# Kernel optimization log

Hardware: AMD Instinct MI355X
Metric: run time of the kernel (lower is better)

## Reference

```python
import math
import jax, jax.numpy as jnp
import numpy as np

ROPE_DIMS = 16  # rope applied to last 16 channels only
N_WIN = 16      # sliding window size


def rmsnorm(x, w):
    return x * jax.lax.rsqrt(jnp.mean(x * x, axis=-1, keepdims=True) + 1e-8) * w


def apply_rope(x, negate=False):
    # x: [B, H, T, C]; rotate last ROPE_DIMS channels with interleaved pairs
    T = x.shape[2]
    x_pass, x_rope = x[..., :-ROPE_DIMS], x[..., -ROPE_DIMS:]
    t = jnp.arange(T, dtype=x.dtype)
    if negate:
        t = -t
    k = jnp.arange(ROPE_DIMS // 2, dtype=x.dtype)
    theta = 10000.0 ** (-2.0 * k / ROPE_DIMS)          # [8]
    freqs = t[:, None] * theta[None, :]                 # [T, 8]
    cos, sin = jnp.cos(freqs), jnp.sin(freqs)
    x1, x2 = x_rope[..., 0::2], x_rope[..., 1::2]
    rx1 = x1 * cos - x2 * sin
    rx2 = x1 * sin + x2 * cos
    rx = jnp.stack([rx1, rx2], axis=-1).reshape(x_rope.shape)
    return jnp.concatenate([x_pass, rx], axis=-1)


def setup_inputs() -> dict:
    key = jax.random.key(0)
    ks = jax.random.split(key, 14)
    B, T, d, c, nh = 4, 2048, 256, 64, 4
    s = 0.02
    return {
        "H": jax.random.normal(ks[0], (B, T, d), jnp.float32),
        "W_Q": jax.random.normal(ks[1], (nh * c, d), jnp.float32) * s,
        "W_K": jax.random.normal(ks[2], (c, d), jnp.float32) * s,
        "W_V": jax.random.normal(ks[3], (c, d), jnp.float32) * s,
        "wq": 1.0 + 0.1 * jax.random.normal(ks[4], (nh, c), jnp.float32),
        "wk": 1.0 + 0.1 * jax.random.normal(ks[5], (c,), jnp.float32),
        "wv": 1.0 + 0.1 * jax.random.normal(ks[6], (c,), jnp.float32),
        "Wg0": jax.random.normal(ks[7], (64, 2 * c), jnp.float32) * s,
        "bg0": jnp.zeros((64,), jnp.float32),
        "Wg1": jax.random.normal(ks[8], (64, 2 * c), jnp.float32) * s,
        "bg1": jnp.zeros((64,), jnp.float32),
        "Wout": jax.random.normal(ks[9], (d, 128), jnp.float32) * s,
        "bout": jnp.zeros((d,), jnp.float32),
    }


def reference(H, W_Q, W_K, W_V, wq, wk, wv, Wg0, bg0, Wg1, bg1, Wout, bout):
    B, T, d = H.shape
    nh, c = wq.shape
    # projections
    Q = (H @ W_Q.T).reshape(B, T, nh, c).transpose(0, 2, 1, 3)   # [B,nh,T,c]
    K = (H @ W_K.T)[:, None]                                      # [B,1,T,c]
    V = (H @ W_V.T)[:, None]                                      # [B,1,T,c]
    # per-head RMSNorm on Q, shared RMSNorm on K/V
    Q = rmsnorm(Q, wq[None, :, None, :])
    K = rmsnorm(K, wk)
    V = rmsnorm(V, wv)
    # partial RoPE (last 16 dims); V is also rotated in this module
    Q = apply_rope(Q)
    K = apply_rope(K)[:, 0]                                       # [B,T,c]
    V = apply_rope(V)[:, 0]
    # dense scores with sliding-window causal mask (width N_WIN)
    S = jnp.einsum('bhtc,bsc->bhts', Q, K) / math.sqrt(c)
    i = jnp.arange(T)[:, None]
    j = jnp.arange(T)[None, :]
    allowed = (j <= i) & (j >= i - (N_WIN - 1))                   # [T,T]
    S = jnp.where(allowed, S, -jnp.inf)
    P = jax.nn.softmax(S, axis=-1)
    O = jnp.einsum('bhts,bsc->bhtc', P, V)                        # [B,nh,T,c]
    O = apply_rope(O, negate=True)
    # group heads {0,1} and {2,3}
    O_g0 = O[:, :2].transpose(0, 2, 1, 3).reshape(B, T, 2 * c)
    O_g1 = O[:, 2:].transpose(0, 2, 1, 3).reshape(B, T, 2 * c)
    p0 = O_g0 @ Wg0.T + bg0
    p1 = O_g1 @ Wg1.T + bg1
    p_all = jnp.concatenate([p0, p1], axis=-1)                    # [B,T,128]
    return p_all @ Wout.T + bout
```

## Files before the change

### kernel.cpp

```cpp
#include <hip/hip_runtime.h>
#include <math.h>

#define T_SEQ 2048
#define DMODEL 256
#define C_HEAD 64
#define NH 4
#define NWIN 16
#define B_SZ 4

typedef __attribute__((ext_vector_type(8))) short bf16x8;
typedef __attribute__((ext_vector_type(8))) unsigned short ushort8;
typedef __attribute__((ext_vector_type(4))) float f32x4;

static __device__ __forceinline__ unsigned short f2bf(float f) {
    union { float f; unsigned int u; } v; v.f = f;
    unsigned int r = v.u + 0x7FFFu + ((v.u >> 16) & 1u);
    return (unsigned short)(r >> 16);
}

__global__ __launch_bounds__(256) void conv_w_kernel(
    const float* __restrict__ WQ, const float* __restrict__ WK,
    const float* __restrict__ WV, const float* __restrict__ Wg0,
    const float* __restrict__ Wg1, const float* __restrict__ Wout,
    unsigned short* __restrict__ dst, float2* __restrict__ rtab) {
    const int tid = threadIdx.x;
    if (blockIdx.x >= 72) {
        const int idx = (blockIdx.x - 72) * 256 + tid;
        const int t = idx >> 3, k = idx & 7;
        const float theta = powf(10000.0f, -0.125f * (float)k);
        const float fr = (float)t * theta;
        rtab[idx] = make_float2(cosf(fr), sinf(fr));
        return;
    }
    const int i = blockIdx.x * 256 + tid;
    const float* s; long off; long doff;
    if (i < 12288) {
        const long e = (long)i * 8;
        const int col = (int)(e >> 8), k = (int)(e & 255);
        if      (col < 256) { s = WQ; off = (long)col * 256 + k; }
        else if (col < 320) { s = WK; off = (long)(col - 256) * 256 + k; }
        else                { s = WV; off = (long)(col - 320) * 256 + k; }
        doff = ((long)(col >> 4) * 8 + (k >> 5)) * 512 + ((k >> 3) & 3) * 128 + (col & 15) * 8;
    } else {
        const long e = (long)(i - 12288) * 8;
        const int col = (int)(e >> 7), k = (int)(e & 127);
        if      (col < 64)  { s = Wg0; off = (long)col * 128 + k; }
        else if (col < 128) { s = Wg1; off = (long)(col - 64) * 128 + k; }
        else                { s = Wout; off = (long)(col - 128) * 128 + k; }
        doff = 98304 + ((long)(col >> 4) * 4 + (k >> 5)) * 512 + ((k >> 3) & 3) * 128 + (col & 15) * 8;
    }
    const float4* s4 = (const float4*)(s + off);
    float4 a = s4[0], b = s4[1];
    ushort8 o;
    o[0] = f2bf(a.x); o[1] = f2bf(a.y); o[2] = f2bf(a.z); o[3] = f2bf(a.w);
    o[4] = f2bf(b.x); o[5] = f2bf(b.y); o[6] = f2bf(b.z); o[7] = f2bf(b.w);
    *(ushort8*)(dst + doff) = o;
}

__global__ __launch_bounds__(512) void fused_kernel(
    const float* __restrict__ H, const unsigned short* __restrict__ Wallb,
    const float* __restrict__ wq, const float* __restrict__ wk,
    const float* __restrict__ wv, const float2* __restrict__ rtab,
    const float* __restrict__ bg0, const float* __restrict__ bg1,
    const float* __restrict__ bout, float* __restrict__ out)
{
    __shared__ __align__(16) char smem[36864];
    char* lds_a = smem;
    char* o_lds = smem;
    char* p_lds = smem + 8192;
    char* q_lds = smem + 16384;
    char* k_lds = smem + 24576;
    char* v_lds = smem + 28672;
    char* p_att = smem + 32768;

    const int tid = threadIdx.x;
    const int blk = blockIdx.x;
    const int b  = blk >> 7;
    const int t0 = (blk & 127) << 4;

    const unsigned short* Wpk2 = Wallb + 98304;

    for (int idx = tid; idx < 1024; idx += 512) {
        int row = idx >> 5, ch = idx & 31;
        int t = t0 - 16 + row; if (t < 0) t = 0;
        const float4* s4 = (const float4*)(H + ((size_t)b * T_SEQ + t) * DMODEL + ch * 8);
        float4 a = s4[0], c = s4[1];
        ushort8 o;
        o[0] = f2bf(a.x); o[1] = f2bf(a.y); o[2] = f2bf(a.z); o[3] = f2bf(a.w);
        o[4] = f2bf(c.x); o[5] = f2bf(c.y); o[6] = f2bf(c.z); o[7] = f2bf(c.w);
        int byte = row * 512 + ch * 16;
        byte ^= (row & 7) << 4;
        *(ushort8*)(lds_a + byte) = o;
    }
    __syncthreads();

    const int w  = tid >> 6;
    const int l  = tid & 63;
    const int g  = l >> 4;
    const int li = l & 15;
    const int lane16 = l * 8;

    if (w < 4) {
        f32x4 acc[4] = {};
        #pragma unroll
        for (int ks = 0; ks < 8; ++ks) {
            const int row = 16 + li;
            int byte = row * 512 + (ks * 32 + g * 8) * 2;
            byte ^= (row & 7) << 4;
            bf16x8 a = *(const bf16x8*)(lds_a + byte);
            #pragma unroll
            for (int nf = 0; nf < 4; ++nf) {
                bf16x8 bq = *(const bf16x8*)(Wallb + (size_t)((w * 4 + nf) * 8 + ks) * 512 + lane16);
                acc[nf] = __builtin_amdgcn_mfma_f32_16x16x32_bf16(a, bq, acc[nf], 0, 0, 0);
            }
        }
        float gw[4];
        #pragma unroll
        for (int nf = 0; nf < 4; ++nf) gw[nf] = wq[w * 64 + nf * 16 + li];
        #pragma unroll
        for (int r = 0; r < 4; ++r) {
            float x0 = acc[0][r], x1 = acc[1][r];
            float x2 = acc[2][r], x3 = acc[3][r];
            float ss = x0 * x0 + x1 * x1 + x2 * x2 + x3 * x3;
            ss += __shfl_xor(ss, 1);
            ss += __shfl_xor(ss, 2);
            ss += __shfl_xor(ss, 4);
            ss += __shfl_xor(ss, 8);
            const float rinv = rsqrtf(ss * (1.0f / 64.0f) + 1e-8f);
            const int tok = g * 4 + r;
            const int t = t0 + tok;
            float v0 = x0 * rinv * gw[0];
            float v1 = x1 * rinv * gw[1];
            float v2 = x2 * rinv * gw[2];
            float v3 = x3 * rinv * gw[3];
            float2 cs = rtab[t * 8 + (li >> 1)];
            float px = __shfl_xor(v3, 1);
            v3 = ((li & 1) == 0) ? (v3 * cs.x - px * cs.y) : (px * cs.y + v3 * cs.x);
            char* qb = q_lds + w * 2048;
            const int sw = (tok & 7) << 4;
            *(unsigned short*)(qb + ((tok * 128 + (0 * 16 + li) * 2) ^ sw)) = f2bf(v0);
            *(unsigned short*)(qb + ((tok * 128 + (1 * 16 + li) * 2) ^ sw)) = f2bf(v1);
            *(unsigned short*)(qb + ((tok * 128 + (2 * 16 + li) * 2) ^ sw)) = f2bf(v2);
            *(unsigned short*)(qb + ((tok * 128 + (3 * 16 + li) * 2) ^ sw)) = f2bf(v3);
        }
    } else {
        const int sel = (w - 4) >> 1;
        const int mfh = (w - 4) & 1;
        f32x4 acc[4] = {};
        #pragma unroll
        for (int ks = 0; ks < 8; ++ks) {
            const int row = mfh * 16 + li;
            int byte = row * 512 + (ks * 32 + g * 8) * 2;
            byte ^= (row & 7) << 4;
            bf16x8 a = *(const bf16x8*)(lds_a + byte);
            #pragma unroll
            for (int nf = 0; nf < 4; ++nf) {
                bf16x8 bkv = *(const bf16x8*)(Wallb + (size_t)((16 + sel * 4 + nf) * 8 + ks) * 512 + lane16);
                acc[nf] = __builtin_amdgcn_mfma_f32_16x16x32_bf16(a, bkv, acc[nf], 0, 0, 0);
            }
        }
        float gw[4];
        #pragma unroll
        for (int nf = 0; nf < 4; ++nf)
            gw[nf] = (sel == 0) ? wk[nf * 16 + li] : wv[nf * 16 + li];
        #pragma unroll
        for (int r = 0; r < 4; ++r) {
            float x0 = acc[0][r], x1 = acc[1][r];
            float x2 = acc[2][r], x3 = acc[3][r];
            float ss = x0 * x0 + x1 * x1 + x2 * x2 + x3 * x3;
            ss += __shfl_xor(ss, 1);
            ss += __shfl_xor(ss, 2);
            ss += __shfl_xor(ss, 4);
            ss += __shfl_xor(ss, 8);
            const float rinv = rsqrtf(ss * (1.0f / 64.0f) + 1e-8f);
            const int row = mfh * 16 + g * 4 + r;
            int tk = t0 - 16 + row; if (tk < 0) tk = 0;
            float v0 = x0 * rinv * gw[0];
            float v1 = x1 * rinv * gw[1];
            float v2 = x2 * rinv * gw[2];
            float v3 = x3 * rinv * gw[3];
            float2 cs = rtab[tk * 8 + (li >> 1)];
            float px = __shfl_xor(v3, 1);
            v3 = ((li & 1) == 0) ? (v3 * cs.x - px * cs.y) : (px * cs.y + v3 * cs.x);
            if (sel == 0) {
                const int sw = (row & 7) << 4;
                *(unsigned short*)(k_lds + ((row * 128 + (0 * 16 + li) * 2) ^ sw)) = f2bf(v0);
                *(unsigned short*)(k_lds + ((row * 128 + (1 * 16 + li) * 2) ^ sw)) = f2bf(v1);
                *(unsigned short*)(k_lds + ((row * 128 + (2 * 16 + li) * 2) ^ sw)) = f2bf(v2);
                *(unsigned short*)(k_lds + ((row * 128 + (3 * 16 + li) * 2) ^ sw)) = f2bf(v3);
            } else {
                const int sw = (row & 12) << 3;
                *(unsigned short*)(v_lds + ((0 * 1024 + row * 32 + li * 2) ^ sw)) = f2bf(v0);
                *(unsigned short*)(v_lds + ((1 * 1024 + row * 32 + li * 2) ^ sw)) = f2bf(v1);
                *(unsigned short*)(v_lds + ((2 * 1024 + row * 32 + li * 2) ^ sw)) = f2bf(v2);
                *(unsigned short*)(v_lds + ((3 * 1024 + row * 32 + li * 2) ^ sw)) = f2bf(v3);
            }
        }
    }
    __syncthreads();

    if (w < 4) {
        const int h = w;
        bf16x8 qf0, qf1;
        {
            const char* qb = q_lds + h * 2048;
            const int sw = (li & 7) << 4;
            qf0 = *(const bf16x8*)(qb + ((li * 128 + g * 16) ^ sw));
            qf1 = *(const bf16x8*)(qb + ((li * 128 + 64 + g * 16) ^ sw));
        }
        f32x4 st[2];
        #pragma unroll
        for (int tile = 0; tile < 2; ++tile) {
            const int row = tile * 16 + li;
            const int sw = (row & 7) << 4;
            bf16x8 kf0 = *(const bf16x8*)(k_lds + ((row * 128 + g * 16) ^ sw));
            bf16x8 kf1 = *(const bf16x8*)(k_lds + ((row * 128 + 64 + g * 16) ^ sw));
            f32x4 acc = {};
            acc = __builtin_amdgcn_mfma_f32_16x16x32_bf16(kf0, qf0, acc, 0, 0, 0);
            acc = __builtin_amdgcn_mfma_f32_16x16x32_bf16(kf1, qf1, acc, 0, 0, 0);
            st[tile] = acc;
        }

        float p[8];
        float mx = -1e30f;
        #pragma unroll
        for (int tile = 0; tile < 2; ++tile) {
            #pragma unroll
            for (int r = 0; r < 4; ++r) {
                int krel = tile * 16 - 16 + g * 4 + r;
                int dd = li - krel;
                bool ok = ((unsigned)dd < 16u) && (t0 + krel >= 0);
                float v = ok ? st[tile][r] * 0.125f : -1e30f;
                p[tile * 4 + r] = v;
                mx = fmaxf(mx, v);
            }
        }
        mx = fmaxf(mx, __shfl_xor(mx, 16));
        mx = fmaxf(mx, __shfl_xor(mx, 32));
        float sum = 0.f;
        #pragma unroll
        for (int i = 0; i < 8; ++i) { p[i] = __expf(p[i] - mx); sum += p[i]; }
        sum += __shfl_xor(sum, 16);
        sum += __shfl_xor(sum, 32);
        const float inv = 1.0f / sum;

        bf16x8 paf;
        {
            char* pbase = p_att + h * 1024;
            uint2 w0, w1;
            w0.x = (unsigned)f2bf(p[0] * inv) | ((unsigned)f2bf(p[1] * inv) << 16);
            w0.y = (unsigned)f2bf(p[2] * inv) | ((unsigned)f2bf(p[3] * inv) << 16);
            w1.x = (unsigned)f2bf(p[4] * inv) | ((unsigned)f2bf(p[5] * inv) << 16);
            w1.y = (unsigned)f2bf(p[6] * inv) | ((unsigned)f2bf(p[7] * inv) << 16);
            const int sw = (li & 3) << 4;
            *(uint2*)(pbase + ((li * 64 + 0 * 32 + g * 8) ^ sw)) = w0;
            *(uint2*)(pbase + ((li * 64 + 1 * 32 + g * 8) ^ sw)) = w1;
            asm volatile("s_waitcnt lgkmcnt(0)" ::: "memory");
            paf = *(const bf16x8*)(pbase + ((li * 64 + g * 16) ^ sw));
        }

        f32x4 o[4] = {};
        #pragma unroll
        for (int ctile = 0; ctile < 4; ++ctile) {
            bf16x8 vf;
            #pragma unroll
            for (int j = 0; j < 8; ++j) {
                int key = g * 8 + j;
                int byte = ctile * 1024 + key * 32 + li * 2;
                byte ^= (key & 12) << 3;
                vf[j] = *(const short*)(v_lds + byte);
            }
            o[ctile] = __builtin_amdgcn_mfma_f32_16x16x32_bf16(paf, vf, o[ctile], 0, 0, 0);
        }

        #pragma unroll
        for (int r = 0; r < 4; ++r) {
            const int row = g * 4 + r;
            const int t = t0 + row;
            float o3 = o[3][r];
            float po = __shfl_xor(o3, 1);
            float2 cs = rtab[t * 8 + (li >> 1)];
            o3 = ((li & 1) == 0) ? (o3 * cs.x + po * cs.y) : (-po * cs.y + o3 * cs.x);
            #pragma unroll
            for (int ctile = 0; ctile < 4; ++ctile) {
                const int col = h * 64 + ctile * 16 + li;
                int byte = row * 512 + col * 2;
                byte ^= (row & 7) << 4;
                float val = (ctile == 3) ? o3 : o[ctile][r];
                *(unsigned short*)(o_lds + byte) = f2bf(val);
            }
        }
    }
    __syncthreads();

    {
        const int gate = w >> 2, colq = w & 3;
        const float* bg = gate ? bg1 : bg0;
        f32x4 accp = {};
        #pragma unroll
        for (int ks = 0; ks < 4; ++ks) {
            int byte = li * 512 + (gate * 128 + ks * 32 + g * 8) * 2;
            byte ^= (li & 7) << 4;
            bf16x8 a = *(const bf16x8*)(o_lds + byte);
            const int colblk = gate * 4 + colq;
            bf16x8 bfr = *(const bf16x8*)(Wpk2 + (size_t)(colblk * 4 + ks) * 512 + lane16);
            accp = __builtin_amdgcn_mfma_f32_16x16x32_bf16(a, bfr, accp, 0, 0, 0);
        }
        const int cl = colq * 16 + li;
        const int pcol = gate * 64 + cl;
        const float bb = bg[cl];
        #pragma unroll
        for (int r = 0; r < 4; ++r) {
            const int row = g * 4 + r;
            int byte = row * 256 + pcol * 2;
            byte ^= (row & 7) << 4;
            *(unsigned short*)(p_lds + byte) = f2bf(accp[r] + bb);
        }
    }
    __syncthreads();

    {
        f32x4 acco[2] = {};
        #pragma unroll
        for (int ks = 0; ks < 4; ++ks) {
            int byte = li * 256 + (ks * 32 + g * 8) * 2;
            byte ^= (li & 7) << 4;
            bf16x8 a = *(const bf16x8*)(p_lds + byte);
            #pragma unroll
            for (int nf = 0; nf < 2; ++nf) {
                const int colblk = 8 + w * 2 + nf;
                bf16x8 bfr = *(const bf16x8*)(Wpk2 + (size_t)(colblk * 4 + ks) * 512 + lane16);
                acco[nf] = __builtin_amdgcn_mfma_f32_16x16x32_bf16(a, bfr, acco[nf], 0, 0, 0);
            }
        }
        #pragma unroll
        for (int nf = 0; nf < 2; ++nf) {
            const int col = w * 32 + nf * 16 + li;
            const float bb = bout[col];
            #pragma unroll
            for (int r = 0; r < 4; ++r) {
                const int row = g * 4 + r;
                out[(size_t)(b * T_SEQ + t0 + row) * DMODEL + col] = acco[nf][r] + bb;
            }
        }
    }
}

extern "C" void kernel_launch(void* const* d_in, const int* in_sizes, int n_in,
                              void* d_out, int out_size, void* d_ws, size_t ws_size,
                              hipStream_t stream) {
    const float* H    = (const float*)d_in[0];
    const float* WQ   = (const float*)d_in[1];
    const float* WK   = (const float*)d_in[2];
    const float* WV   = (const float*)d_in[3];
    const float* wq   = (const float*)d_in[4];
    const float* wk   = (const float*)d_in[5];
    const float* wv   = (const float*)d_in[6];
    const float* Wg0  = (const float*)d_in[7];
    const float* bg0  = (const float*)d_in[8];
    const float* Wg1  = (const float*)d_in[9];
    const float* bg1  = (const float*)d_in[10];
    const float* Wout = (const float*)d_in[11];
    const float* bout = (const float*)d_in[12];
    float* out = (float*)d_out;

    char* ws = (char*)d_ws;
    unsigned short* Wallb = (unsigned short*)ws;
    float2* rtab = (float2*)(ws + 294912);

    conv_w_kernel<<<136, 256, 0, stream>>>(WQ, WK, WV, Wg0, Wg1, Wout, Wallb, rtab);
    fused_kernel<<<B_SZ * T_SEQ / 16, 512, 0, stream>>>(H, Wallb, wq, wk, wv, rtab,
                                                        bg0, bg1, bout, out);
}
```

Baseline: 22.77 us.

## Double tokens per block to 32 and store V transposed for vector loads

Each block now processes 32 tokens with 1024 threads, so the 16-token halo of H loads and K/V projections is shared across more queries. V is written to LDS in a transposed, padded layout so attention fragments are read as one 16-byte vector instead of eight scalar gathers. Warp roles are remapped across all stages. The trade-off is half as many blocks, larger LDS use and lower occupancy per CU, with two idle waves during projection.

```diff
diff --git a/kernel.cpp b/kernel.cpp
--- a/kernel.cpp
+++ b/kernel.cpp
@@ -57,30 +57,30 @@
     *(ushort8*)(dst + doff) = o;
 }
 
-__global__ __launch_bounds__(512) void fused_kernel(
+__global__ __launch_bounds__(1024) void fused_kernel(
     const float* __restrict__ H, const unsigned short* __restrict__ Wallb,
     const float* __restrict__ wq, const float* __restrict__ wk,
     const float* __restrict__ wv, const float2* __restrict__ rtab,
     const float* __restrict__ bg0, const float* __restrict__ bg1,
     const float* __restrict__ bout, float* __restrict__ out)
 {
-    __shared__ __align__(16) char smem[36864];
+    __shared__ __align__(16) char smem[62464];
     char* lds_a = smem;
     char* o_lds = smem;
-    char* p_lds = smem + 8192;
-    char* q_lds = smem + 16384;
-    char* k_lds = smem + 24576;
-    char* v_lds = smem + 28672;
-    char* p_att = smem + 32768;
+    char* p_lds = smem + 16384;
+    char* q_lds = smem + 24576;
+    char* k_lds = smem + 40960;
+    char* v_t   = smem + 47104;
+    char* p_att = smem + 54272;
 
     const int tid = threadIdx.x;
     const int blk = blockIdx.x;
-    const int b  = blk >> 7;
-    const int t0 = (blk & 127) << 4;
+    const int b  = blk >> 6;
+    const int t0 = (blk & 63) << 5;
 
     const unsigned short* Wpk2 = Wallb + 98304;
 
-    for (int idx = tid; idx < 1024; idx += 512) {
+    for (int idx = tid; idx < 1536; idx += 1024) {
         int row = idx >> 5, ch = idx & 31;
         int t = t0 - 16 + row; if (t < 0) t = 0;
         const float4* s4 = (const float4*)(H + ((size_t)b * T_SEQ + t) * DMODEL + ch * 8);
@@ -100,23 +100,25 @@
     const int li = l & 15;
     const int lane16 = l * 8;
 
-    if (w < 4) {
+    if (w < 8) {
+        const int h  = w >> 1;
+        const int th = w & 1;
         f32x4 acc[4] = {};
         #pragma unroll
         for (int ks = 0; ks < 8; ++ks) {
-            const int row = 16 + li;
+            const int row = 16 + th * 16 + li;
             int byte = row * 512 + (ks * 32 + g * 8) * 2;
             byte ^= (row & 7) << 4;
             bf16x8 a = *(const bf16x8*)(lds_a + byte);
             #pragma unroll
             for (int nf = 0; nf < 4; ++nf) {
-                bf16x8 bq = *(const bf16x8*)(Wallb + (size_t)((w * 4 + nf) * 8 + ks) * 512 + lane16);
+                bf16x8 bq = *(const bf16x8*)(Wallb + (size_t)((h * 4 + nf) * 8 + ks) * 512 + lane16);
                 acc[nf] = __builtin_amdgcn_mfma_f32_16x16x32_bf16(a, bq, acc[nf], 0, 0, 0);
             }
         }
         float gw[4];
         #pragma unroll
-        for (int nf = 0; nf < 4; ++nf) gw[nf] = wq[w * 64 + nf * 16 + li];
+        for (int nf = 0; nf < 4; ++nf) gw[nf] = wq[h * 64 + nf * 16 + li];
         #pragma unroll
         for (int r = 0; r < 4; ++r) {
             float x0 = acc[0][r], x1 = acc[1][r];
@@ -127,7 +129,7 @@
             ss += __shfl_xor(ss, 4);
             ss += __shfl_xor(ss, 8);
             const float rinv = rsqrtf(ss * (1.0f / 64.0f) + 1e-8f);
-            const int tok = g * 4 + r;
+            const int tok = th * 16 + g * 4 + r;
             const int t = t0 + tok;
             float v0 = x0 * rinv * gw[0];
             float v1 = x1 * rinv * gw[1];
@@ -136,20 +138,21 @@
             float2 cs = rtab[t * 8 + (li >> 1)];
             float px = __shfl_xor(v3, 1);
             v3 = ((li & 1) == 0) ? (v3 * cs.x - px * cs.y) : (px * cs.y + v3 * cs.x);
-            char* qb = q_lds + w * 2048;
+            char* qb = q_lds + h * 4096;
             const int sw = (tok & 7) << 4;
             *(unsigned short*)(qb + ((tok * 128 + (0 * 16 + li) * 2) ^ sw)) = f2bf(v0);
             *(unsigned short*)(qb + ((tok * 128 + (1 * 16 + li) * 2) ^ sw)) = f2bf(v1);
             *(unsigned short*)(qb + ((tok * 128 + (2 * 16 + li) * 2) ^ sw)) = f2bf(v2);
             *(unsigned short*)(qb + ((tok * 128 + (3 * 16 + li) * 2) ^ sw)) = f2bf(v3);
         }
-    } else {
-        const int sel = (w - 4) >> 1;
-        const int mfh = (w - 4) & 1;
+    } else if (w < 14) {
+        const int idx  = w - 8;
+        const int sel  = (idx >= 3) ? 1 : 0;
+        const int slab = sel ? (idx - 3) : idx;
         f32x4 acc[4] = {};
         #pragma unroll
         for (int ks = 0; ks < 8; ++ks) {
-            const int row = mfh * 16 + li;
+            const int row = slab * 16 + li;
             int byte = row * 512 + (ks * 32 + g * 8) * 2;
             byte ^= (row & 7) << 4;
             bf16x8 a = *(const bf16x8*)(lds_a + byte);
@@ -173,7 +176,7 @@
             ss += __shfl_xor(ss, 4);
             ss += __shfl_xor(ss, 8);
             const float rinv = rsqrtf(ss * (1.0f / 64.0f) + 1e-8f);
-            const int row = mfh * 16 + g * 4 + r;
+            const int row = slab * 16 + g * 4 + r;
             int tk = t0 - 16 + row; if (tk < 0) tk = 0;
             float v0 = x0 * rinv * gw[0];
             float v1 = x1 * rinv * gw[1];
@@ -189,29 +192,30 @@
                 *(unsigned short*)(k_lds + ((row * 128 + (2 * 16 + li) * 2) ^ sw)) = f2bf(v2);
                 *(unsigned short*)(k_lds + ((row * 128 + (3 * 16 + li) * 2) ^ sw)) = f2bf(v3);
             } else {
-                const int sw = (row & 12) << 3;
-                *(unsigned short*)(v_lds + ((0 * 1024 + row * 32 + li * 2) ^ sw)) = f2bf(v0);
-                *(unsigned short*)(v_lds + ((1 * 1024 + row * 32 + li * 2) ^ sw)) = f2bf(v1);
-                *(unsigned short*)(v_lds + ((2 * 1024 + row * 32 + li * 2) ^ sw)) = f2bf(v2);
-                *(unsigned short*)(v_lds + ((3 * 1024 + row * 32 + li * 2) ^ sw)) = f2bf(v3);
+                *(unsigned short*)(v_t + (0 * 16 + li) * 112 + row * 2) = f2bf(v0);
+                *(unsigned short*)(v_t + (1 * 16 + li) * 112 + row * 2) = f2bf(v1);
+                *(unsigned short*)(v_t + (2 * 16 + li) * 112 + row * 2) = f2bf(v2);
+                *(unsigned short*)(v_t + (3 * 16 + li) * 112 + row * 2) = f2bf(v3);
             }
         }
     }
     __syncthreads();
 
-    if (w < 4) {
-        const int h = w;
+    if (w < 8) {
+        const int h  = w >> 1;
+        const int th = w & 1;
         bf16x8 qf0, qf1;
         {
-            const char* qb = q_lds + h * 2048;
-            const int sw = (li & 7) << 4;
-            qf0 = *(const bf16x8*)(qb + ((li * 128 + g * 16) ^ sw));
-            qf1 = *(const bf16x8*)(qb + ((li * 128 + 64 + g * 16) ^ sw));
+            const char* qb = q_lds + h * 4096;
+            const int tok = th * 16 + li;
+            const int sw = (tok & 7) << 4;
+            qf0 = *(const bf16x8*)(qb + ((tok * 128 + g * 16) ^ sw));
+            qf1 = *(const bf16x8*)(qb + ((tok * 128 + 64 + g * 16) ^ sw));
         }
         f32x4 st[2];
         #pragma unroll
         for (int tile = 0; tile < 2; ++tile) {
-            const int row = tile * 16 + li;
+            const int row = th * 16 + tile * 16 + li;
             const int sw = (row & 7) << 4;
             bf16x8 kf0 = *(const bf16x8*)(k_lds + ((row * 128 + g * 16) ^ sw));
             bf16x8 kf1 = *(const bf16x8*)(k_lds + ((row * 128 + 64 + g * 16) ^ sw));
@@ -229,7 +233,7 @@
             for (int r = 0; r < 4; ++r) {
                 int krel = tile * 16 - 16 + g * 4 + r;
                 int dd = li - krel;
-                bool ok = ((unsigned)dd < 16u) && (t0 + krel >= 0);
+                bool ok = ((unsigned)dd < 16u) && (t0 + th * 16 + krel >= 0);
                 float v = ok ? st[tile][r] * 0.125f : -1e30f;
                 p[tile * 4 + r] = v;
                 mx = fmaxf(mx, v);
@@ -246,7 +250,7 @@
 
         bf16x8 paf;
         {
-            char* pbase = p_att + h * 1024;
+            char* pbase = p_att + w * 1024;
             uint2 w0, w1;
             w0.x = (unsigned)f2bf(p[0] * inv) | ((unsigned)f2bf(p[1] * inv) << 16);
             w0.y = (unsigned)f2bf(p[2] * inv) | ((unsigned)f2bf(p[3] * inv) << 16);
@@ -262,20 +266,13 @@
         f32x4 o[4] = {};
         #pragma unroll
         for (int ctile = 0; ctile < 4; ++ctile) {
-            bf16x8 vf;
-            #pragma unroll
-            for (int j = 0; j < 8; ++j) {
-                int key = g * 8 + j;
-                int byte = ctile * 1024 + key * 32 + li * 2;
-                byte ^= (key & 12) << 3;
-                vf[j] = *(const short*)(v_lds + byte);
-            }
+            bf16x8 vf = *(const bf16x8*)(v_t + (ctile * 16 + li) * 112 + th * 32 + g * 16);
             o[ctile] = __builtin_amdgcn_mfma_f32_16x16x32_bf16(paf, vf, o[ctile], 0, 0, 0);
         }
 
         #pragma unroll
         for (int r = 0; r < 4; ++r) {
-            const int row = g * 4 + r;
+            const int row = th * 16 + g * 4 + r;
             const int t = t0 + row;
             float o3 = o[3][r];
             float po = __shfl_xor(o3, 1);
@@ -294,13 +291,14 @@
     __syncthreads();
 
     {
-        const int gate = w >> 2, colq = w & 3;
+        const int gate = (w >> 3) & 1, colq = (w >> 1) & 3, rh = w & 1;
         const float* bg = gate ? bg1 : bg0;
         f32x4 accp = {};
         #pragma unroll
         for (int ks = 0; ks < 4; ++ks) {
-            int byte = li * 512 + (gate * 128 + ks * 32 + g * 8) * 2;
-            byte ^= (li & 7) << 4;
+            const int row = rh * 16 + li;
+            int byte = row * 512 + (gate * 128 + ks * 32 + g * 8) * 2;
+            byte ^= (row & 7) << 4;
             bf16x8 a = *(const bf16x8*)(o_lds + byte);
             const int colblk = gate * 4 + colq;
             bf16x8 bfr = *(const bf16x8*)(Wpk2 + (size_t)(colblk * 4 + ks) * 512 + lane16);
@@ -311,7 +309,7 @@
         const float bb = bg[cl];
         #pragma unroll
         for (int r = 0; r < 4; ++r) {
-            const int row = g * 4 + r;
+            const int row = rh * 16 + g * 4 + r;
             int byte = row * 256 + pcol * 2;
             byte ^= (row & 7) << 4;
             *(unsigned short*)(p_lds + byte) = f2bf(accp[r] + bb);
@@ -323,24 +321,27 @@
         f32x4 acco[2] = {};
         #pragma unroll
         for (int ks = 0; ks < 4; ++ks) {
-            int byte = li * 256 + (ks * 32 + g * 8) * 2;
-            byte ^= (li & 7) << 4;
-            bf16x8 a = *(const bf16x8*)(p_lds + byte);
-            #pragma unroll
-            for (int nf = 0; nf < 2; ++nf) {
-                const int colblk = 8 + w * 2 + nf;
-                bf16x8 bfr = *(const bf16x8*)(Wpk2 + (size_t)(colblk * 4 + ks) * 512 + lane16);
-                acco[nf] = __builtin_amdgcn_mfma_f32_16x16x32_bf16(a, bfr, acco[nf], 0, 0, 0);
-            }
-        }
-        #pragma unroll
-        for (int nf = 0; nf < 2; ++nf) {
-            const int col = w * 32 + nf * 16 + li;
-            const float bb = bout[col];
+            bf16x8 a[2];
+            #pragma unroll
+            for (int mf = 0; mf < 2; ++mf) {
+                const int row = mf * 16 + li;
+                int byte = row * 256 + (ks * 32 + g * 8) * 2;
+                byte ^= (row & 7) << 4;
+                a[mf] = *(const bf16x8*)(p_lds + byte);
+            }
+            const int colblk = 8 + w;
+            bf16x8 bfr = *(const bf16x8*)(Wpk2 + (size_t)(colblk * 4 + ks) * 512 + lane16);
+            acco[0] = __builtin_amdgcn_mfma_f32_16x16x32_bf16(a[0], bfr, acco[0], 0, 0, 0);
+            acco[1] = __builtin_amdgcn_mfma_f32_16x16x32_bf16(a[1], bfr, acco[1], 0, 0, 0);
+        }
+        const int col = w * 16 + li;
+        const float bb = bout[col];
+        #pragma unroll
+        for (int mf = 0; mf < 2; ++mf) {
             #pragma unroll
             for (int r = 0; r < 4; ++r) {
-                const int row = g * 4 + r;
-                out[(size_t)(b * T_SEQ + t0 + row) * DMODEL + col] = acco[nf][r] + bb;
+                const int row = mf * 16 + g * 4 + r;
+                out[(size_t)(b * T_SEQ + t0 + row) * DMODEL + col] = acco[mf][r] + bb;
             }
         }
     }
@@ -369,6 +370,6 @@
     float2* rtab = (float2*)(ws + 294912);
 
     conv_w_kernel<<<136, 256, 0, stream>>>(WQ, WK, WV, Wg0, Wg1, Wout, Wallb, rtab);
-    fused_kernel<<<B_SZ * T_SEQ / 16, 512, 0, stream>>>(H, Wallb, wq, wk, wv, rtab,
-                                                        bg0, bg1, bout, out);
+    fused_kernel<<<B_SZ * T_SEQ / 32, 1024, 0, stream>>>(H, Wallb, wq, wk, wv, rtab,
+                                                         bg0, bg1, bout, out);
 }
```

After: 22.11 us. -2.9%, faster.

## Process two 16-token tiles per block with software-pipelined stages

Applied to the files above, without the earlier changes.

Each block now handles two consecutive 16-token tiles in separate LDS contexts. The stages are staggered so one tile's QKV projection overlaps the other's attention, gates and output, and the global H load for the second tile is issued before the first tile's QKV. V is stored transposed with padding so the PV MFMA operand comes from one vector read instead of eight scalar reads. This halves the grid to 256 blocks and doubles LDS use, which may reduce occupancy and leave some CUs idle.

```diff
diff --git a/kernel.cpp b/kernel.cpp
--- a/kernel.cpp
+++ b/kernel.cpp
@@ -64,35 +64,16 @@
     const float* __restrict__ bg0, const float* __restrict__ bg1,
     const float* __restrict__ bout, float* __restrict__ out)
 {
-    __shared__ __align__(16) char smem[36864];
-    char* lds_a = smem;
-    char* o_lds = smem;
-    char* p_lds = smem + 8192;
-    char* q_lds = smem + 16384;
-    char* k_lds = smem + 24576;
-    char* v_lds = smem + 28672;
-    char* p_att = smem + 32768;
-
+    __shared__ __align__(16) char smem[75776];
     const int tid = threadIdx.x;
     const int blk = blockIdx.x;
-    const int b  = blk >> 7;
-    const int t0 = (blk & 127) << 4;
+    const int b   = blk >> 6;
+    const int t0A = (blk & 63) << 5;
+    const int t0B = t0A + 16;
+    char* ctxA = smem;
+    char* ctxB = smem + 37888;
 
     const unsigned short* Wpk2 = Wallb + 98304;
-
-    for (int idx = tid; idx < 1024; idx += 512) {
-        int row = idx >> 5, ch = idx & 31;
-        int t = t0 - 16 + row; if (t < 0) t = 0;
-        const float4* s4 = (const float4*)(H + ((size_t)b * T_SEQ + t) * DMODEL + ch * 8);
-        float4 a = s4[0], c = s4[1];
-        ushort8 o;
-        o[0] = f2bf(a.x); o[1] = f2bf(a.y); o[2] = f2bf(a.z); o[3] = f2bf(a.w);
-        o[4] = f2bf(c.x); o[5] = f2bf(c.y); o[6] = f2bf(c.z); o[7] = f2bf(c.w);
-        int byte = row * 512 + ch * 16;
-        byte ^= (row & 7) << 4;
-        *(ushort8*)(lds_a + byte) = o;
-    }
-    __syncthreads();
 
     const int w  = tid >> 6;
     const int l  = tid & 63;
@@ -100,106 +81,142 @@
     const int li = l & 15;
     const int lane16 = l * 8;
 
-    if (w < 4) {
-        f32x4 acc[4] = {};
-        #pragma unroll
-        for (int ks = 0; ks < 8; ++ks) {
-            const int row = 16 + li;
-            int byte = row * 512 + (ks * 32 + g * 8) * 2;
+    auto stage_load = [&](int t0, float4 sb[2][2]) {
+        #pragma unroll
+        for (int it = 0; it < 2; ++it) {
+            const int idx = tid + it * 512;
+            const int row = idx >> 5, ch = idx & 31;
+            int t = t0 - 16 + row; if (t < 0) t = 0;
+            const float4* s4 = (const float4*)(H + ((size_t)b * T_SEQ + t) * DMODEL + ch * 8);
+            sb[it][0] = s4[0];
+            sb[it][1] = s4[1];
+        }
+    };
+    auto stage_write = [&](char* ctx, float4 sb[2][2]) {
+        #pragma unroll
+        for (int it = 0; it < 2; ++it) {
+            const int idx = tid + it * 512;
+            const int row = idx >> 5, ch = idx & 31;
+            ushort8 o;
+            o[0] = f2bf(sb[it][0].x); o[1] = f2bf(sb[it][0].y);
+            o[2] = f2bf(sb[it][0].z); o[3] = f2bf(sb[it][0].w);
+            o[4] = f2bf(sb[it][1].x); o[5] = f2bf(sb[it][1].y);
+            o[6] = f2bf(sb[it][1].z); o[7] = f2bf(sb[it][1].w);
+            int byte = row * 512 + ch * 16;
             byte ^= (row & 7) << 4;
-            bf16x8 a = *(const bf16x8*)(lds_a + byte);
-            #pragma unroll
-            for (int nf = 0; nf < 4; ++nf) {
-                bf16x8 bq = *(const bf16x8*)(Wallb + (size_t)((w * 4 + nf) * 8 + ks) * 512 + lane16);
-                acc[nf] = __builtin_amdgcn_mfma_f32_16x16x32_bf16(a, bq, acc[nf], 0, 0, 0);
-            }
-        }
-        float gw[4];
-        #pragma unroll
-        for (int nf = 0; nf < 4; ++nf) gw[nf] = wq[w * 64 + nf * 16 + li];
-        #pragma unroll
-        for (int r = 0; r < 4; ++r) {
-            float x0 = acc[0][r], x1 = acc[1][r];
-            float x2 = acc[2][r], x3 = acc[3][r];
-            float ss = x0 * x0 + x1 * x1 + x2 * x2 + x3 * x3;
-            ss += __shfl_xor(ss, 1);
-            ss += __shfl_xor(ss, 2);
-            ss += __shfl_xor(ss, 4);
-            ss += __shfl_xor(ss, 8);
-            const float rinv = rsqrtf(ss * (1.0f / 64.0f) + 1e-8f);
-            const int tok = g * 4 + r;
-            const int t = t0 + tok;
-            float v0 = x0 * rinv * gw[0];
-            float v1 = x1 * rinv * gw[1];
-            float v2 = x2 * rinv * gw[2];
-            float v3 = x3 * rinv * gw[3];
-            float2 cs = rtab[t * 8 + (li >> 1)];
-            float px = __shfl_xor(v3, 1);
-            v3 = ((li & 1) == 0) ? (v3 * cs.x - px * cs.y) : (px * cs.y + v3 * cs.x);
-            char* qb = q_lds + w * 2048;
-            const int sw = (tok & 7) << 4;
-            *(unsigned short*)(qb + ((tok * 128 + (0 * 16 + li) * 2) ^ sw)) = f2bf(v0);
-            *(unsigned short*)(qb + ((tok * 128 + (1 * 16 + li) * 2) ^ sw)) = f2bf(v1);
-            *(unsigned short*)(qb + ((tok * 128 + (2 * 16 + li) * 2) ^ sw)) = f2bf(v2);
-            *(unsigned short*)(qb + ((tok * 128 + (3 * 16 + li) * 2) ^ sw)) = f2bf(v3);
-        }
-    } else {
-        const int sel = (w - 4) >> 1;
-        const int mfh = (w - 4) & 1;
-        f32x4 acc[4] = {};
-        #pragma unroll
-        for (int ks = 0; ks < 8; ++ks) {
-            const int row = mfh * 16 + li;
-            int byte = row * 512 + (ks * 32 + g * 8) * 2;
-            byte ^= (row & 7) << 4;
-            bf16x8 a = *(const bf16x8*)(lds_a + byte);
-            #pragma unroll
-            for (int nf = 0; nf < 4; ++nf) {
-                bf16x8 bkv = *(const bf16x8*)(Wallb + (size_t)((16 + sel * 4 + nf) * 8 + ks) * 512 + lane16);
-                acc[nf] = __builtin_amdgcn_mfma_f32_16x16x32_bf16(a, bkv, acc[nf], 0, 0, 0);
-            }
-        }
-        float gw[4];
-        #pragma unroll
-        for (int nf = 0; nf < 4; ++nf)
-            gw[nf] = (sel == 0) ? wk[nf * 16 + li] : wv[nf * 16 + li];
-        #pragma unroll
-        for (int r = 0; r < 4; ++r) {
-            float x0 = acc[0][r], x1 = acc[1][r];
-            float x2 = acc[2][r], x3 = acc[3][r];
-            float ss = x0 * x0 + x1 * x1 + x2 * x2 + x3 * x3;
-            ss += __shfl_xor(ss, 1);
-            ss += __shfl_xor(ss, 2);
-            ss += __shfl_xor(ss, 4);
-            ss += __shfl_xor(ss, 8);
-            const float rinv = rsqrtf(ss * (1.0f / 64.0f) + 1e-8f);
-            const int row = mfh * 16 + g * 4 + r;
-            int tk = t0 - 16 + row; if (tk < 0) tk = 0;
-            float v0 = x0 * rinv * gw[0];
-            float v1 = x1 * rinv * gw[1];
-            float v2 = x2 * rinv * gw[2];
-            float v3 = x3 * rinv * gw[3];
-            float2 cs = rtab[tk * 8 + (li >> 1)];
-            float px = __shfl_xor(v3, 1);
-            v3 = ((li & 1) == 0) ? (v3 * cs.x - px * cs.y) : (px * cs.y + v3 * cs.x);
-            if (sel == 0) {
-                const int sw = (row & 7) << 4;
-                *(unsigned short*)(k_lds + ((row * 128 + (0 * 16 + li) * 2) ^ sw)) = f2bf(v0);
-                *(unsigned short*)(k_lds + ((row * 128 + (1 * 16 + li) * 2) ^ sw)) = f2bf(v1);
-                *(unsigned short*)(k_lds + ((row * 128 + (2 * 16 + li) * 2) ^ sw)) = f2bf(v2);
-                *(unsigned short*)(k_lds + ((row * 128 + (3 * 16 + li) * 2) ^ sw)) = f2bf(v3);
-            } else {
-                const int sw = (row & 12) << 3;
-                *(unsigned short*)(v_lds + ((0 * 1024 + row * 32 + li * 2) ^ sw)) = f2bf(v0);
-                *(unsigned short*)(v_lds + ((1 * 1024 + row * 32 + li * 2) ^ sw)) = f2bf(v1);
-                *(unsigned short*)(v_lds + ((2 * 1024 + row * 32 + li * 2) ^ sw)) = f2bf(v2);
-                *(unsigned short*)(v_lds + ((3 * 1024 + row * 32 + li * 2) ^ sw)) = f2bf(v3);
-            }
-        }
-    }
-    __syncthreads();
-
-    if (w < 4) {
+            *(ushort8*)(ctx + byte) = o;
+        }
+    };
+
+    auto qkv = [&](char* ctx, int t0) {
+        char* q_lds = ctx + 16384;
+        char* k_lds = ctx + 24576;
+        char* v_t   = ctx + 28672;
+        if (w < 4) {
+            f32x4 acc[4] = {};
+            #pragma unroll
+            for (int ks = 0; ks < 8; ++ks) {
+                const int row = 16 + li;
+                int byte = row * 512 + (ks * 32 + g * 8) * 2;
+                byte ^= (row & 7) << 4;
+                bf16x8 a = *(const bf16x8*)(ctx + byte);
+                #pragma unroll
+                for (int nf = 0; nf < 4; ++nf) {
+                    bf16x8 bq = *(const bf16x8*)(Wallb + (size_t)((w * 4 + nf) * 8 + ks) * 512 + lane16);
+                    acc[nf] = __builtin_amdgcn_mfma_f32_16x16x32_bf16(a, bq, acc[nf], 0, 0, 0);
+                }
+            }
+            float gw[4];
+            #pragma unroll
+            for (int nf = 0; nf < 4; ++nf) gw[nf] = wq[w * 64 + nf * 16 + li];
+            #pragma unroll
+            for (int r = 0; r < 4; ++r) {
+                float x0 = acc[0][r], x1 = acc[1][r];
+                float x2 = acc[2][r], x3 = acc[3][r];
+                float ss = x0 * x0 + x1 * x1 + x2 * x2 + x3 * x3;
+                ss += __shfl_xor(ss, 1);
+                ss += __shfl_xor(ss, 2);
+                ss += __shfl_xor(ss, 4);
+                ss += __shfl_xor(ss, 8);
+                const float rinv = rsqrtf(ss * (1.0f / 64.0f) + 1e-8f);
+                const int tok = g * 4 + r;
+                const int t = t0 + tok;
+                float v0 = x0 * rinv * gw[0];
+                float v1 = x1 * rinv * gw[1];
+                float v2 = x2 * rinv * gw[2];
+                float v3 = x3 * rinv * gw[3];
+                float2 cs = rtab[t * 8 + (li >> 1)];
+                float px = __shfl_xor(v3, 1);
+                v3 = ((li & 1) == 0) ? (v3 * cs.x - px * cs.y) : (px * cs.y + v3 * cs.x);
+                char* qb = q_lds + w * 2048;
+                const int sw = (tok & 7) << 4;
+                *(unsigned short*)(qb + ((tok * 128 + (0 * 16 + li) * 2) ^ sw)) = f2bf(v0);
+                *(unsigned short*)(qb + ((tok * 128 + (1 * 16 + li) * 2) ^ sw)) = f2bf(v1);
+                *(unsigned short*)(qb + ((tok * 128 + (2 * 16 + li) * 2) ^ sw)) = f2bf(v2);
+                *(unsigned short*)(qb + ((tok * 128 + (3 * 16 + li) * 2) ^ sw)) = f2bf(v3);
+            }
+        } else {
+            const int sel = (w - 4) >> 1;
+            const int mfh = (w - 4) & 1;
+            f32x4 acc[4] = {};
+            #pragma unroll
+            for (int ks = 0; ks < 8; ++ks) {
+                const int row = mfh * 16 + li;
+                int byte = row * 512 + (ks * 32 + g * 8) * 2;
+                byte ^= (row & 7) << 4;
+                bf16x8 a = *(const bf16x8*)(ctx + byte);
+                #pragma unroll
+                for (int nf = 0; nf < 4; ++nf) {
+                    bf16x8 bkv = *(const bf16x8*)(Wallb + (size_t)((16 + sel * 4 + nf) * 8 + ks) * 512 + lane16);
+                    acc[nf] = __builtin_amdgcn_mfma_f32_16x16x32_bf16(a, bkv, acc[nf], 0, 0, 0);
+                }
+            }
+            float gw[4];
+            #pragma unroll
+            for (int nf = 0; nf < 4; ++nf)
+                gw[nf] = (sel == 0) ? wk[nf * 16 + li] : wv[nf * 16 + li];
+            #pragma unroll
+            for (int r = 0; r < 4; ++r) {
+                float x0 = acc[0][r], x1 = acc[1][r];
+                float x2 = acc[2][r], x3 = acc[3][r];
+                float ss = x0 * x0 + x1 * x1 + x2 * x2 + x3 * x3;
+                ss += __shfl_xor(ss, 1);
+                ss += __shfl_xor(ss, 2);
+                ss += __shfl_xor(ss, 4);
+                ss += __shfl_xor(ss, 8);
+                const float rinv = rsqrtf(ss * (1.0f / 64.0f) + 1e-8f);
+                const int row = mfh * 16 + g * 4 + r;
+                int tk = t0 - 16 + row; if (tk < 0) tk = 0;
+                float v0 = x0 * rinv * gw[0];
+                float v1 = x1 * rinv * gw[1];
+                float v2 = x2 * rinv * gw[2];
+                float v3 = x3 * rinv * gw[3];
+                float2 cs = rtab[tk * 8 + (li >> 1)];
+                float px = __shfl_xor(v3, 1);
+                v3 = ((li & 1) == 0) ? (v3 * cs.x - px * cs.y) : (px * cs.y + v3 * cs.x);
+                if (sel == 0) {
+                    const int sw = (row & 7) << 4;
+                    *(unsigned short*)(k_lds + ((row * 128 + (0 * 16 + li) * 2) ^ sw)) = f2bf(v0);
+                    *(unsigned short*)(k_lds + ((row * 128 + (1 * 16 + li) * 2) ^ sw)) = f2bf(v1);
+                    *(unsigned short*)(k_lds + ((row * 128 + (2 * 16 + li) * 2) ^ sw)) = f2bf(v2);
+                    *(unsigned short*)(k_lds + ((row * 128 + (3 * 16 + li) * 2) ^ sw)) = f2bf(v3);
+                } else {
+                    *(unsigned short*)(v_t + (0 * 16 + li) * 80 + row * 2) = f2bf(v0);
+                    *(unsigned short*)(v_t + (1 * 16 + li) * 80 + row * 2) = f2bf(v1);
+                    *(unsigned short*)(v_t + (2 * 16 + li) * 80 + row * 2) = f2bf(v2);
+                    *(unsigned short*)(v_t + (3 * 16 + li) * 80 + row * 2) = f2bf(v3);
+                }
+            }
+        }
+    };
+
+    auto attn = [&](char* ctx, int t0) {
+        if (w >= 4) return;
+        char* o_lds = ctx;
+        char* q_lds = ctx + 16384;
+        char* k_lds = ctx + 24576;
+        char* v_t   = ctx + 28672;
+        char* p_att = ctx + 33792;
         const int h = w;
         bf16x8 qf0, qf1;
         {
@@ -220,7 +237,6 @@
             acc = __builtin_amdgcn_mfma_f32_16x16x32_bf16(kf1, qf1, acc, 0, 0, 0);
             st[tile] = acc;
         }
-
         float p[8];
         float mx = -1e30f;
         #pragma unroll
@@ -262,14 +278,7 @@
         f32x4 o[4] = {};
         #pragma unroll
         for (int ctile = 0; ctile < 4; ++ctile) {
-            bf16x8 vf;
-            #pragma unroll
-            for (int j = 0; j < 8; ++j) {
-                int key = g * 8 + j;
-                int byte = ctile * 1024 + key * 32 + li * 2;
-                byte ^= (key & 12) << 3;
-                vf[j] = *(const short*)(v_lds + byte);
-            }
+            bf16x8 vf = *(const bf16x8*)(v_t + (ctile * 16 + li) * 80 + g * 16);
             o[ctile] = __builtin_amdgcn_mfma_f32_16x16x32_bf16(paf, vf, o[ctile], 0, 0, 0);
         }
 
@@ -290,10 +299,11 @@
                 *(unsigned short*)(o_lds + byte) = f2bf(val);
             }
         }
-    }
-    __syncthreads();
-
-    {
+    };
+
+    auto gates = [&](char* ctx) {
+        char* o_lds = ctx;
+        char* p_lds = ctx + 8192;
         const int gate = w >> 2, colq = w & 3;
         const float* bg = gate ? bg1 : bg0;
         f32x4 accp = {};
@@ -316,10 +326,10 @@
             byte ^= (row & 7) << 4;
             *(unsigned short*)(p_lds + byte) = f2bf(accp[r] + bb);
         }
-    }
-    __syncthreads();
-
-    {
+    };
+
+    auto outp = [&](char* ctx, int t0) {
+        char* p_lds = ctx + 8192;
         f32x4 acco[2] = {};
         #pragma unroll
         for (int ks = 0; ks < 4; ++ks) {
@@ -343,7 +353,26 @@
                 out[(size_t)(b * T_SEQ + t0 + row) * DMODEL + col] = acco[nf][r] + bb;
             }
         }
-    }
+    };
+
+    float4 sb[2][2];
+    stage_load(t0A, sb);
+    stage_write(ctxA, sb);
+    __syncthreads();
+    stage_load(t0B, sb);
+    qkv(ctxA, t0A);
+    stage_write(ctxB, sb);
+    __syncthreads();
+    attn(ctxA, t0A);
+    qkv(ctxB, t0B);
+    __syncthreads();
+    gates(ctxA);
+    attn(ctxB, t0B);
+    __syncthreads();
+    outp(ctxA, t0A);
+    gates(ctxB);
+    __syncthreads();
+    outp(ctxB, t0B);
 }
 
 extern "C" void kernel_launch(void* const* d_in, const int* in_sizes, int n_in,
@@ -369,6 +398,6 @@
     float2* rtab = (float2*)(ws + 294912);
 
     conv_w_kernel<<<136, 256, 0, stream>>>(WQ, WK, WV, Wg0, Wg1, Wout, Wallb, rtab);
-    fused_kernel<<<B_SZ * T_SEQ / 16, 512, 0, stream>>>(H, Wallb, wq, wk, wv, rtab,
+    fused_kernel<<<B_SZ * T_SEQ / 32, 512, 0, stream>>>(H, Wallb, wq, wk, wv, rtab,
                                                         bg0, bg1, bout, out);
 }
```

Measured after the change: 25.10 us. 1.1x slower.

## Prefetch weight fragments across barriers and store V transposed in LDS

Applied to the files above, without the earlier changes.

Weight fragments for the projection GEMM are now software-pipelined two k-steps ahead. Gate and output weights are loaded before the barriers so global latency overlaps with other work, and the projection loop is unified across warps. V is stored transposed with a padded stride, so each PV fragment is a single 16-byte LDS load instead of eight scalar loads. __syncthreads is replaced by an inline-asm waitcnt lgkmcnt plus s_barrier, which raises register pressure and depends on vmcnt not needing to drain for LDS correctness.

```diff
diff --git a/kernel.cpp b/kernel.cpp
--- a/kernel.cpp
+++ b/kernel.cpp
@@ -11,6 +11,8 @@
 typedef __attribute__((ext_vector_type(8))) short bf16x8;
 typedef __attribute__((ext_vector_type(8))) unsigned short ushort8;
 typedef __attribute__((ext_vector_type(4))) float f32x4;
+
+#define BAR() asm volatile("s_waitcnt lgkmcnt(0)\n\ts_barrier" ::: "memory")
 
 static __device__ __forceinline__ unsigned short f2bf(float f) {
     union { float f; unsigned int u; } v; v.f = f;
@@ -64,14 +66,14 @@
     const float* __restrict__ bg0, const float* __restrict__ bg1,
     const float* __restrict__ bout, float* __restrict__ out)
 {
-    __shared__ __align__(16) char smem[36864];
+    __shared__ __align__(16) char smem[37888];
     char* lds_a = smem;
     char* o_lds = smem;
     char* p_lds = smem + 8192;
     char* q_lds = smem + 16384;
     char* k_lds = smem + 24576;
-    char* v_lds = smem + 28672;
-    char* p_att = smem + 32768;
+    char* v_t   = smem + 28672;
+    char* p_att = smem + 33792;
 
     const int tid = threadIdx.x;
     const int blk = blockIdx.x;
@@ -79,6 +81,19 @@
     const int t0 = (blk & 127) << 4;
 
     const unsigned short* Wpk2 = Wallb + 98304;
+
+    const int w  = tid >> 6;
+    const int l  = tid & 63;
+    const int g  = l >> 4;
+    const int li = l & 15;
+    const int lane16 = l * 8;
+
+    const int cb0  = (w < 4) ? (w * 4) : (16 + ((w - 4) >> 1) * 4);
+    const int rowa = (w < 4) ? (16 + li) : (((w - 4) & 1) * 16 + li);
+    const int sel  = (w - 4) >> 1;
+    const int mfh  = (w - 4) & 1;
+
+#define WFRAG(nf, ks) (*(const bf16x8*)(Wallb + (size_t)((cb0 + (nf)) * 8 + (ks)) * 512 + lane16))
 
     for (int idx = tid; idx < 1024; idx += 512) {
         int row = idx >> 5, ch = idx & 31;
@@ -92,28 +107,30 @@
         byte ^= (row & 7) << 4;
         *(ushort8*)(lds_a + byte) = o;
     }
-    __syncthreads();
-
-    const int w  = tid >> 6;
-    const int l  = tid & 63;
-    const int g  = l >> 4;
-    const int li = l & 15;
-    const int lane16 = l * 8;
+    bf16x8 cur[4], nxt[4];
+    #pragma unroll
+    for (int nf = 0; nf < 4; ++nf) { cur[nf] = WFRAG(nf, 0); nxt[nf] = WFRAG(nf, 1); }
+    BAR();
+
+    f32x4 acc[4] = {};
+    #pragma unroll
+    for (int ks = 0; ks < 8; ++ks) {
+        bf16x8 fut[4];
+        if (ks < 6) {
+            #pragma unroll
+            for (int nf = 0; nf < 4; ++nf) fut[nf] = WFRAG(nf, ks + 2);
+        }
+        int abyte = rowa * 512 + (ks * 32 + g * 8) * 2;
+        abyte ^= (rowa & 7) << 4;
+        bf16x8 a = *(const bf16x8*)(lds_a + abyte);
+        #pragma unroll
+        for (int nf = 0; nf < 4; ++nf)
+            acc[nf] = __builtin_amdgcn_mfma_f32_16x16x32_bf16(a, cur[nf], acc[nf], 0, 0, 0);
+        #pragma unroll
+        for (int nf = 0; nf < 4; ++nf) { cur[nf] = nxt[nf]; nxt[nf] = fut[nf]; }
+    }
 
     if (w < 4) {
-        f32x4 acc[4] = {};
-        #pragma unroll
-        for (int ks = 0; ks < 8; ++ks) {
-            const int row = 16 + li;
-            int byte = row * 512 + (ks * 32 + g * 8) * 2;
-            byte ^= (row & 7) << 4;
-            bf16x8 a = *(const bf16x8*)(lds_a + byte);
-            #pragma unroll
-            for (int nf = 0; nf < 4; ++nf) {
-                bf16x8 bq = *(const bf16x8*)(Wallb + (size_t)((w * 4 + nf) * 8 + ks) * 512 + lane16);
-                acc[nf] = __builtin_amdgcn_mfma_f32_16x16x32_bf16(a, bq, acc[nf], 0, 0, 0);
-            }
-        }
         float gw[4];
         #pragma unroll
         for (int nf = 0; nf < 4; ++nf) gw[nf] = wq[w * 64 + nf * 16 + li];
@@ -144,21 +161,6 @@
             *(unsigned short*)(qb + ((tok * 128 + (3 * 16 + li) * 2) ^ sw)) = f2bf(v3);
         }
     } else {
-        const int sel = (w - 4) >> 1;
-        const int mfh = (w - 4) & 1;
-        f32x4 acc[4] = {};
-        #pragma unroll
-        for (int ks = 0; ks < 8; ++ks) {
-            const int row = mfh * 16 + li;
-            int byte = row * 512 + (ks * 32 + g * 8) * 2;
-            byte ^= (row & 7) << 4;
-            bf16x8 a = *(const bf16x8*)(lds_a + byte);
-            #pragma unroll
-            for (int nf = 0; nf < 4; ++nf) {
-                bf16x8 bkv = *(const bf16x8*)(Wallb + (size_t)((16 + sel * 4 + nf) * 8 + ks) * 512 + lane16);
-                acc[nf] = __builtin_amdgcn_mfma_f32_16x16x32_bf16(a, bkv, acc[nf], 0, 0, 0);
-            }
-        }
         float gw[4];
         #pragma unroll
         for (int nf = 0; nf < 4; ++nf)
@@ -189,16 +191,22 @@
                 *(unsigned short*)(k_lds + ((row * 128 + (2 * 16 + li) * 2) ^ sw)) = f2bf(v2);
                 *(unsigned short*)(k_lds + ((row * 128 + (3 * 16 + li) * 2) ^ sw)) = f2bf(v3);
             } else {
-                const int sw = (row & 12) << 3;
-                *(unsigned short*)(v_lds + ((0 * 1024 + row * 32 + li * 2) ^ sw)) = f2bf(v0);
-                *(unsigned short*)(v_lds + ((1 * 1024 + row * 32 + li * 2) ^ sw)) = f2bf(v1);
-                *(unsigned short*)(v_lds + ((2 * 1024 + row * 32 + li * 2) ^ sw)) = f2bf(v2);
-                *(unsigned short*)(v_lds + ((3 * 1024 + row * 32 + li * 2) ^ sw)) = f2bf(v3);
+                *(unsigned short*)(v_t + (0 * 16 + li) * 80 + row * 2) = f2bf(v0);
+                *(unsigned short*)(v_t + (1 * 16 + li) * 80 + row * 2) = f2bf(v1);
+                *(unsigned short*)(v_t + (2 * 16 + li) * 80 + row * 2) = f2bf(v2);
+                *(unsigned short*)(v_t + (3 * 16 + li) * 80 + row * 2) = f2bf(v3);
             }
         }
     }
-    __syncthreads();
-
+    BAR();
+
+    const int gate = w >> 2, colq = w & 3;
+    bf16x8 gpre[4];
+    if (w >= 4) {
+        #pragma unroll
+        for (int ks = 0; ks < 4; ++ks)
+            gpre[ks] = *(const bf16x8*)(Wpk2 + (size_t)((gate * 4 + colq) * 4 + ks) * 512 + lane16);
+    }
     if (w < 4) {
         const int h = w;
         bf16x8 qf0, qf1;
@@ -215,10 +223,10 @@
             const int sw = (row & 7) << 4;
             bf16x8 kf0 = *(const bf16x8*)(k_lds + ((row * 128 + g * 16) ^ sw));
             bf16x8 kf1 = *(const bf16x8*)(k_lds + ((row * 128 + 64 + g * 16) ^ sw));
-            f32x4 acc = {};
-            acc = __builtin_amdgcn_mfma_f32_16x16x32_bf16(kf0, qf0, acc, 0, 0, 0);
-            acc = __builtin_amdgcn_mfma_f32_16x16x32_bf16(kf1, qf1, acc, 0, 0, 0);
-            st[tile] = acc;
+            f32x4 sa = {};
+            sa = __builtin_amdgcn_mfma_f32_16x16x32_bf16(kf0, qf0, sa, 0, 0, 0);
+            sa = __builtin_amdgcn_mfma_f32_16x16x32_bf16(kf1, qf1, sa, 0, 0, 0);
+            st[tile] = sa;
         }
 
         float p[8];
@@ -262,14 +270,7 @@
         f32x4 o[4] = {};
         #pragma unroll
         for (int ctile = 0; ctile < 4; ++ctile) {
-            bf16x8 vf;
-            #pragma unroll
-            for (int j = 0; j < 8; ++j) {
-                int key = g * 8 + j;
-                int byte = ctile * 1024 + key * 32 + li * 2;
-                byte ^= (key & 12) << 3;
-                vf[j] = *(const short*)(v_lds + byte);
-            }
+            bf16x8 vf = *(const bf16x8*)(v_t + (ctile * 16 + li) * 80 + g * 16);
             o[ctile] = __builtin_amdgcn_mfma_f32_16x16x32_bf16(paf, vf, o[ctile], 0, 0, 0);
         }
 
@@ -290,11 +291,14 @@
                 *(unsigned short*)(o_lds + byte) = f2bf(val);
             }
         }
-    }
-    __syncthreads();
-
+        #pragma unroll
+        for (int ks = 0; ks < 4; ++ks)
+            gpre[ks] = *(const bf16x8*)(Wpk2 + (size_t)((gate * 4 + colq) * 4 + ks) * 512 + lane16);
+    }
+    BAR();
+
+    bf16x8 opre[2][4];
     {
-        const int gate = w >> 2, colq = w & 3;
         const float* bg = gate ? bg1 : bg0;
         f32x4 accp = {};
         #pragma unroll
@@ -302,10 +306,13 @@
             int byte = li * 512 + (gate * 128 + ks * 32 + g * 8) * 2;
             byte ^= (li & 7) << 4;
             bf16x8 a = *(const bf16x8*)(o_lds + byte);
-            const int colblk = gate * 4 + colq;
-            bf16x8 bfr = *(const bf16x8*)(Wpk2 + (size_t)(colblk * 4 + ks) * 512 + lane16);
-            accp = __builtin_amdgcn_mfma_f32_16x16x32_bf16(a, bfr, accp, 0, 0, 0);
-        }
+            accp = __builtin_amdgcn_mfma_f32_16x16x32_bf16(a, gpre[ks], accp, 0, 0, 0);
+        }
+        #pragma unroll
+        for (int nf = 0; nf < 2; ++nf)
+            #pragma unroll
+            for (int ks = 0; ks < 4; ++ks)
+                opre[nf][ks] = *(const bf16x8*)(Wpk2 + (size_t)((8 + w * 2 + nf) * 4 + ks) * 512 + lane16);
         const int cl = colq * 16 + li;
         const int pcol = gate * 64 + cl;
         const float bb = bg[cl];
@@ -317,7 +324,7 @@
             *(unsigned short*)(p_lds + byte) = f2bf(accp[r] + bb);
         }
     }
-    __syncthreads();
+    BAR();
 
     {
         f32x4 acco[2] = {};
@@ -327,11 +334,8 @@
             byte ^= (li & 7) << 4;
             bf16x8 a = *(const bf16x8*)(p_lds + byte);
             #pragma unroll
-            for (int nf = 0; nf < 2; ++nf) {
-                const int colblk = 8 + w * 2 + nf;
-                bf16x8 bfr = *(const bf16x8*)(Wpk2 + (size_t)(colblk * 4 + ks) * 512 + lane16);
-                acco[nf] = __builtin_amdgcn_mfma_f32_16x16x32_bf16(a, bfr, acco[nf], 0, 0, 0);
-            }
+            for (int nf = 0; nf < 2; ++nf)
+                acco[nf] = __builtin_amdgcn_mfma_f32_16x16x32_bf16(a, opre[nf][ks], acco[nf], 0, 0, 0);
         }
         #pragma unroll
         for (int nf = 0; nf < 2; ++nf) {
@@ -344,6 +348,7 @@
             }
         }
     }
+#undef WFRAG
 }
 
 extern "C" void kernel_launch(void* const* d_in, const int* in_sizes, int n_in,
```

After: 22.38 us. About the same (-1.7%).
